# Kernel optimization log

Measured on AMD Instinct MI355X. Metric: run time of the kernel, lower is better.

The kernel has to match this reference:

```python
import jax, jax.numpy as jnp
import numpy as np

TEMPS = (0.02, 0.05, 0.2)
EPS = 1e-06


def _pairwise_dist_sq(x, y):
    # (N, M) squared L2 distances, clamped at 0 like the torch version
    dsq = (x * x).sum(-1)[:, None] + (y * y).sum(-1)[None, :] - 2.0 * (x @ y.T)
    return jnp.maximum(dsq, 0.0)


def reference(gen_features, pos_features, drift_scales):
    gen, pos = gen_features, pos_features
    N = gen.shape[0]
    # Distances are temperature-independent; compute once and reuse across temps.
    d_att = jnp.sqrt(_pairwise_dist_sq(gen, pos))  # (N_gen, N_pos)
    eye = jnp.eye(N, dtype=bool)
    dsq_rep = _pairwise_dist_sq(gen, gen)
    # diagonal gets masked to -inf in the logits anyway; replace 0 before sqrt for numerical safety
    d_rep = jnp.sqrt(jnp.where(eye, 1.0, dsq_rep))  # (N_gen, N_gen)

    drift_sum = jnp.zeros_like(gen)
    for i, T in enumerate(TEMPS):
        # attraction: sum_j softmax(-d/T)_ij * (pos_j - gen_i) == softmax @ pos - gen
        # (weights sum to 1 along axis=1, so the -gen_i term factors out)
        w_att = jax.nn.softmax(-d_att / T, axis=1)
        attraction = w_att @ pos - gen
        # repulsion: self-pair excluded via -inf logit (masked_fill(inf) on distances)
        logits_rep = jnp.where(eye, -jnp.inf, -d_rep / T)
        w_rep = jax.nn.softmax(logits_rep, axis=1)
        repulsion = w_rep @ gen - gen
        scale = jnp.maximum(drift_scales[i], EPS)
        drift_sum = drift_sum + (attraction - repulsion) / scale
    return drift_sum / len(TEMPS)


def setup_inputs() -> dict:
    key = jax.random.key(0)
    k1, k2 = jax.random.split(key)
    return {
        "gen_features": jax.random.normal(k1, (8192, 1024), dtype=jnp.float32),
        "pos_features": jax.random.normal(k2, (8192, 1024), dtype=jnp.float32),
        "drift_scales": jnp.ones((3,), dtype=jnp.float32),
    }
```

## Files before the change

kernel.cpp:

```cpp
#include <hip/hip_runtime.h>
#include <hip/hip_bf16.h>

#define NN 8192
#define DD 1024
#define KK 16384

using half8 = __attribute__((ext_vector_type(8))) _Float16;
using half4 = __attribute__((ext_vector_type(4))) _Float16;
using f32x4 = __attribute__((ext_vector_type(4))) float;

__device__ __align__(16) _Float16 g_gh[(size_t)NN * DD];
__device__ __align__(16) _Float16 g_ph[(size_t)NN * DD];
__device__ __align__(16) _Float16 g_vt[(size_t)DD * KK];
__device__ float g_gn[NN];
__device__ float g_pn[NN];
__device__ float g_datt[(size_t)NN * NN];
__device__ float g_drep[(size_t)NN * NN];
__device__ __align__(16) _Float16 g_w[(size_t)NN * KK];
__device__ float g_part[2 * (size_t)NN * DD];

typedef const __attribute__((address_space(1))) void GV;
typedef __attribute__((address_space(3))) void LV;
__device__ inline void gload16(const void* g, void* l) {
    __builtin_amdgcn_global_load_lds((GV*)g, (LV*)l, 16, 0, 0);
}

__global__ __launch_bounds__(256) void k_conv(const float* __restrict__ gen,
                                              const float* __restrict__ pos) {
    int b = blockIdx.x;
    int r = b & (NN - 1);
    const float* src = (b < NN) ? gen : pos;
    _Float16* dsth = (b < NN) ? g_gh : g_ph;
    float* dstn = (b < NN) ? g_gn : g_pn;
    int t = threadIdx.x;
    const float4* s4 = (const float4*)(src + (size_t)r * DD);
    float4 x = s4[t];
    half4 h = {(_Float16)x.x, (_Float16)x.y, (_Float16)x.z, (_Float16)x.w};
    *(half4*)(dsth + (size_t)r * DD + t * 4) = h;
    float s = x.x * x.x + x.y * x.y + x.z * x.z + x.w * x.w;
#pragma unroll
    for (int off = 32; off; off >>= 1) s += __shfl_xor(s, off);
    __shared__ float red[4];
    if ((t & 63) == 0) red[t >> 6] = s;
    __syncthreads();
    if (t == 0) dstn[r] = red[0] + red[1] + red[2] + red[3];
}

__global__ __launch_bounds__(256) void k_tr(const float* __restrict__ pos,
                                            const float* __restrict__ gen) {
    int jt = blockIdx.x;
    int dt = blockIdx.y;
    int z = blockIdx.z;
    const float* src = z ? gen : pos;
    size_t cbase = z ? (size_t)NN : 0;
    __shared__ _Float16 tile[64][68];
    int t = threadIdx.x;
    int j0 = jt * 64, d0 = dt * 64;
#pragma unroll
    for (int p = 0; p < 4; p++) {
        int idx = t + p * 256;
        int r = idx >> 4;
        int c4 = idx & 15;
        float4 x = *(const float4*)(src + (size_t)(j0 + r) * DD + d0 + c4 * 4);
        tile[r][c4 * 4 + 0] = (_Float16)x.x;
        tile[r][c4 * 4 + 1] = (_Float16)x.y;
        tile[r][c4 * 4 + 2] = (_Float16)x.z;
        tile[r][c4 * 4 + 3] = (_Float16)x.w;
    }
    __syncthreads();
#pragma unroll
    for (int p = 0; p < 4; p++) {
        int idx = t + p * 256;
        int d = idx >> 4;
        int j4 = idx & 15;
        half4 h = {tile[j4 * 4 + 0][d], tile[j4 * 4 + 1][d],
                   tile[j4 * 4 + 2][d], tile[j4 * 4 + 3][d]};
        *(half4*)(g_vt + (size_t)(d0 + d) * KK + cbase + j0 + j4 * 4) = h;
    }
}

#define MFMA16(A_, B_, C_) __builtin_amdgcn_mfma_f32_16x16x32_f16(A_, B_, C_, 0, 0, 0)
#define BAR() __builtin_amdgcn_s_barrier()
#define LGKM0() do { asm volatile("s_waitcnt lgkmcnt(0)" ::: "memory"); \
                     __builtin_amdgcn_sched_barrier(0); } while (0)
#define VM4() asm volatile("s_waitcnt vmcnt(4)" ::: "memory")
#define VM0() asm volatile("s_waitcnt vmcnt(0)" ::: "memory")

template <int LDK>
__device__ inline void gemm_core(const _Float16* __restrict__ A,
                                 const _Float16* __restrict__ B,
                                 int arow0, int brow0, int kcol0, int ntiles,
                                 _Float16* lds, f32x4 acc[8][4]) {
    int t = threadIdx.x;
    int w = t >> 6, lane = t & 63;
    int wm = w >> 2, wn = w & 3;
    int q = lane >> 4, li = lane & 15;
    _Float16* sA = lds;
    _Float16* sB = lds + 4 * 8192;

    int offA[8], offB[4];
#pragma unroll
    for (int m = 0; m < 8; ++m) {
        int row = wm * 128 + m * 16 + li;
        offA[m] = row * 32 + (q ^ ((row >> 1) & 3)) * 8;
    }
#pragma unroll
    for (int n = 0; n < 4; ++n) {
        int row = wn * 64 + n * 16 + li;
        offB[n] = row * 32 + (q ^ ((row >> 1) & 3)) * 8;
    }

    int rbase = w * 16 + (lane >> 2);
    int csrc = (lane & 3) ^ ((rbase >> 1) & 3);
    const _Float16* gA0 = A + (size_t)(arow0 + rbase) * LDK + kcol0 + csrc * 8;
    const _Float16* gA1 = gA0 + (size_t)128 * LDK;
    const _Float16* gB0 = B + (size_t)(brow0 + rbase) * LDK + kcol0 + csrc * 8;
    const _Float16* gB1 = gB0 + (size_t)128 * LDK;
    int ldst = w * 512;

#define STAGE_A(tile_) do { \
    gload16(gA0 + (size_t)(tile_) * 32, sA + ((tile_) & 3) * 8192 + ldst); \
    gload16(gA1 + (size_t)(tile_) * 32, sA + ((tile_) & 3) * 8192 + 4096 + ldst); } while (0)
#define STAGE_B(tile_) do { \
    gload16(gB0 + (size_t)(tile_) * 32, sB + ((tile_) & 3) * 8192 + ldst); \
    gload16(gB1 + (size_t)(tile_) * 32, sB + ((tile_) & 3) * 8192 + 4096 + ldst); } while (0)

    STAGE_A(0); STAGE_B(0); STAGE_A(1); STAGE_B(1);
    VM4();
    BAR();

    int nwin = ntiles >> 1;
    half8 af[4], bf[4], af2[4];
#pragma unroll 2
    for (int wi = 0; wi < nwin; ++wi) {
        int t0 = 2 * wi, t1 = t0 + 1;
        const _Float16* a0 = sA + (t0 & 3) * 8192;
        const _Float16* b0 = sB + (t0 & 3) * 8192;
        const _Float16* a1 = sA + (t1 & 3) * 8192;
        const _Float16* b1 = sB + (t1 & 3) * 8192;
#pragma unroll
        for (int m = 0; m < 4; ++m) af[m] = *(const half8*)(a0 + offA[m]);
#pragma unroll
        for (int n = 0; n < 4; ++n) bf[n] = *(const half8*)(b0 + offB[n]);
        if (t0 + 2 < ntiles) STAGE_A(t0 + 2);
        BAR();
        LGKM0();
        __builtin_amdgcn_s_setprio(1);
#pragma unroll
        for (int m = 0; m < 4; ++m)
#pragma unroll
            for (int n = 0; n < 4; ++n)
                acc[m][n] = MFMA16(af[m], bf[n], acc[m][n]);
        __builtin_amdgcn_s_setprio(0);
        BAR();
#pragma unroll
        for (int m = 0; m < 4; ++m) af2[m] = *(const half8*)(a0 + offA[m + 4]);
        if (t0 + 2 < ntiles) STAGE_B(t0 + 2);
        BAR();
        LGKM0();
        __builtin_amdgcn_s_setprio(1);
#pragma unroll
        for (int m = 0; m < 4; ++m)
#pragma unroll
            for (int n = 0; n < 4; ++n)
                acc[m + 4][n] = MFMA16(af2[m], bf[n], acc[m + 4][n]);
        __builtin_amdgcn_s_setprio(0);
        if (wi < nwin - 1) VM4(); else VM0();
        BAR();
#pragma unroll
        for (int m = 0; m < 4; ++m) af[m] = *(const half8*)(a1 + offA[m]);
#pragma unroll
        for (int n = 0; n < 4; ++n) bf[n] = *(const half8*)(b1 + offB[n]);
        if (t1 + 2 < ntiles) STAGE_A(t1 + 2);
        BAR();
        LGKM0();
        __builtin_amdgcn_s_setprio(1);
#pragma unroll
        for (int m = 0; m < 4; ++m)
#pragma unroll
            for (int n = 0; n < 4; ++n)
                acc[m][n] = MFMA16(af[m], bf[n], acc[m][n]);
        __builtin_amdgcn_s_setprio(0);
        BAR();
#pragma unroll
        for (int m = 0; m < 4; ++m) af2[m] = *(const half8*)(a1 + offA[m + 4]);
        if (t1 + 2 < ntiles) STAGE_B(t1 + 2);
        BAR();
        LGKM0();
        __builtin_amdgcn_s_setprio(1);
#pragma unroll
        for (int m = 0; m < 4; ++m)
#pragma unroll
            for (int n = 0; n < 4; ++n)
                acc[m + 4][n] = MFMA16(af2[m], bf[n], acc[m + 4][n]);
        __builtin_amdgcn_s_setprio(0);
        if (wi < nwin - 1) {
            VM4();
            BAR();
        }
    }
#undef STAGE_A
#undef STAGE_B
}

__global__ __launch_bounds__(512, 2) void k_qk2() {
    extern __shared__ _Float16 lds[];
    int id = blockIdx.y * 32 + blockIdx.x;
    id = (id & 7) * 128 + (id >> 3);
    int rt = id >> 5, ct = id & 31;
    int rep = blockIdx.z;
    const _Float16* A = g_gh;
    const _Float16* B = rep ? g_gh : g_ph;
    const float* An = g_gn;
    const float* Bn = rep ? g_gn : g_pn;
    float* outp = rep ? g_drep : g_datt;

    f32x4 acc[8][4] = {};
    gemm_core<DD>(A, B, rt * 256, ct * 256, 0, DD / 32, lds, acc);

    int t = threadIdx.x, w = t >> 6, lane = t & 63;
    int wm = w >> 2, wn = w & 3, q = lane >> 4, li = lane & 15;
    float bnv[4];
#pragma unroll
    for (int n = 0; n < 4; ++n) bnv[n] = Bn[ct * 256 + wn * 64 + n * 16 + li];
#pragma unroll
    for (int m = 0; m < 8; ++m) {
        int gi0 = rt * 256 + wm * 128 + m * 16 + q * 4;
#pragma unroll
        for (int r = 0; r < 4; ++r) {
            int gi = gi0 + r;
            float an = An[gi];
            float* orow = outp + (size_t)gi * NN;
#pragma unroll
            for (int n = 0; n < 4; ++n) {
                int gj = ct * 256 + wn * 64 + n * 16 + li;
                float dsq = an + bnv[n] - 2.0f * acc[m][n][r];
                float d = sqrtf(fmaxf(dsq, 0.0f));
                if (rep && gi == gj) d = 1e30f;
                orow[gj] = d;
            }
        }
    }
}

__global__ __launch_bounds__(256) void k_sw(const float* __restrict__ scales) {
    int i = blockIdx.x, t = threadIdx.x;
    const float4* ra = (const float4*)(g_datt + (size_t)i * NN);
    const float4* rr = (const float4*)(g_drep + (size_t)i * NN);
    float va[32], vr[32];
    float mna = 1e30f, mnr = 1e30f;
#pragma unroll
    for (int p = 0; p < 8; ++p) {
        float4 x = ra[t + p * 256];
        float4 y = rr[t + p * 256];
        va[p * 4 + 0] = x.x; va[p * 4 + 1] = x.y; va[p * 4 + 2] = x.z; va[p * 4 + 3] = x.w;
        vr[p * 4 + 0] = y.x; vr[p * 4 + 1] = y.y; vr[p * 4 + 2] = y.z; vr[p * 4 + 3] = y.w;
        mna = fminf(mna, fminf(fminf(x.x, x.y), fminf(x.z, x.w)));
        mnr = fminf(mnr, fminf(fminf(y.x, y.y), fminf(y.z, y.w)));
    }
#pragma unroll
    for (int off = 32; off; off >>= 1) {
        mna = fminf(mna, __shfl_xor(mna, off));
        mnr = fminf(mnr, __shfl_xor(mnr, off));
    }
    __shared__ float sm[2][4];
    __shared__ float ss[6][4];
    int wv = t >> 6;
    if ((t & 63) == 0) { sm[0][wv] = mna; sm[1][wv] = mnr; }
    __syncthreads();
    mna = fminf(fminf(sm[0][0], sm[0][1]), fminf(sm[0][2], sm[0][3]));
    mnr = fminf(fminf(sm[1][0], sm[1][1]), fminf(sm[1][2], sm[1][3]));
    float s0 = 0.f, s1 = 0.f, s2 = 0.f, s3 = 0.f, s4 = 0.f, s5 = 0.f;
#pragma unroll
    for (int k = 0; k < 32; ++k) {
        float da = va[k] - mna;
        s0 += __expf(da * -50.0f); s1 += __expf(da * -20.0f); s2 += __expf(da * -5.0f);
        float dr = vr[k] - mnr;
        s3 += __expf(dr * -50.0f); s4 += __expf(dr * -20.0f); s5 += __expf(dr * -5.0f);
    }
#pragma unroll
    for (int off = 32; off; off >>= 1) {
        s0 += __shfl_xor(s0, off); s1 += __shfl_xor(s1, off); s2 += __shfl_xor(s2, off);
        s3 += __shfl_xor(s3, off); s4 += __shfl_xor(s4, off); s5 += __shfl_xor(s5, off);
    }
    if ((t & 63) == 0) {
        ss[0][wv] = s0; ss[1][wv] = s1; ss[2][wv] = s2;
        ss[3][wv] = s3; ss[4][wv] = s4; ss[5][wv] = s5;
    }
    __syncthreads();
    float l0 = ss[0][0] + ss[0][1] + ss[0][2] + ss[0][3];
    float l1 = ss[1][0] + ss[1][1] + ss[1][2] + ss[1][3];
    float l2 = ss[2][0] + ss[2][1] + ss[2][2] + ss[2][3];
    float l3 = ss[3][0] + ss[3][1] + ss[3][2] + ss[3][3];
    float l4 = ss[4][0] + ss[4][1] + ss[4][2] + ss[4][3];
    float l5 = ss[5][0] + ss[5][1] + ss[5][2] + ss[5][3];
    float i0 = 1.0f / (3.0f * fmaxf(scales[0], 1e-6f));
    float i1 = 1.0f / (3.0f * fmaxf(scales[1], 1e-6f));
    float i2 = 1.0f / (3.0f * fmaxf(scales[2], 1e-6f));
    float ca0 = i0 / l0, ca1 = i1 / l1, ca2 = i2 / l2;
    float cr0 = -i0 / l3, cr1 = -i1 / l4, cr2 = -i2 / l5;
    _Float16* wa = g_w + (size_t)i * KK;
    _Float16* wr = wa + NN;
#pragma unroll
    for (int p = 0; p < 8; ++p) {
        half4 ha, hr;
#pragma unroll
        for (int qq = 0; qq < 4; ++qq) {
            float da = va[p * 4 + qq] - mna;
            ha[qq] = (_Float16)(ca0 * __expf(da * -50.0f) + ca1 * __expf(da * -20.0f) +
                                ca2 * __expf(da * -5.0f));
            float dr = vr[p * 4 + qq] - mnr;
            hr[qq] = (_Float16)(cr0 * __expf(dr * -50.0f) + cr1 * __expf(dr * -20.0f) +
                                cr2 * __expf(dr * -5.0f));
        }
        *(half4*)(wa + (size_t)(t + p * 256) * 4) = ha;
        *(half4*)(wr + (size_t)(t + p * 256) * 4) = hr;
    }
}

__global__ __launch_bounds__(512, 2) void k_gemm2() {
    extern __shared__ _Float16 lds[];
    int id = blockIdx.y * 4 + blockIdx.x;
    id = (id & 7) * 16 + (id >> 3);
    int rt = id >> 2, ct = id & 3;
    int z = blockIdx.z;
    f32x4 acc[8][4] = {};
    gemm_core<KK>(g_w, g_vt, rt * 256, ct * 256, z * (KK / 2), (KK / 2) / 32, lds, acc);
    float* outp = g_part + (size_t)z * NN * DD;
    int t = threadIdx.x, w = t >> 6, lane = t & 63;
    int wm = w >> 2, wn = w & 3, q = lane >> 4, li = lane & 15;
#pragma unroll
    for (int m = 0; m < 8; ++m) {
#pragma unroll
        for (int r = 0; r < 4; ++r) {
            int gi = rt * 256 + wm * 128 + m * 16 + q * 4 + r;
            float* orow = outp + (size_t)gi * DD;
#pragma unroll
            for (int n = 0; n < 4; ++n) {
                int gj = ct * 256 + wn * 64 + n * 16 + li;
                orow[gj] = acc[m][n][r];
            }
        }
    }
}

__global__ __launch_bounds__(256) void k_red(float* __restrict__ out) {
    size_t base = (size_t)blockIdx.x * 256 + threadIdx.x;
    const float4* p0 = (const float4*)g_part;
    const float4* p1 = (const float4*)(g_part + (size_t)NN * DD);
    float4* o4 = (float4*)out;
#pragma unroll
    for (int p = 0; p < 4; ++p) {
        size_t idx = base + (size_t)p * 524288;
        float4 a = p0[idx], b = p1[idx];
        float4 c = {a.x + b.x, a.y + b.y, a.z + b.z, a.w + b.w};
        o4[idx] = c;
    }
}

extern "C" void kernel_launch(void* const* d_in, const int* in_sizes, int n_in,
                              void* d_out, int out_size, void* d_ws, size_t ws_size,
                              hipStream_t stream) {
    (void)in_sizes; (void)n_in; (void)d_ws; (void)ws_size; (void)out_size;
    const float* gen = (const float*)d_in[0];
    const float* pos = (const float*)d_in[1];
    const float* scales = (const float*)d_in[2];

    hipFuncSetAttribute((const void*)k_qk2, hipFuncAttributeMaxDynamicSharedMemorySize, 131072);
    hipFuncSetAttribute((const void*)k_gemm2, hipFuncAttributeMaxDynamicSharedMemorySize, 131072);

    k_conv<<<dim3(2 * NN), 256, 0, stream>>>(gen, pos);
    k_tr<<<dim3(128, 16, 2), 256, 0, stream>>>(pos, gen);
    k_qk2<<<dim3(32, 32, 2), 512, 131072, stream>>>();
    k_sw<<<dim3(NN), 256, 0, stream>>>(scales);
    k_gemm2<<<dim3(4, 32, 2), 512, 131072, stream>>>();
    k_red<<<dim3(2048), 256, 0, stream>>>((float*)d_out);
}
```

Baseline: 898.3 us.

## Store distance matrices as 16-bit fixed point staged through LDS with nontemporal stores

The distance matrices passed between the QK kernel and the softmax-weight kernel are now quantized to unsigned 16-bit fixed point (scale 1024) instead of fp32. This halves the dominant intermediate traffic of two 8192x8192 matrices. The tiles are staged in LDS so global writes become coalesced 16-byte rows. The weight kernel reads and writes with wider vectors and nontemporal hints. The quantization adds rounding of about 1/2048 on distances, and values above about 64 saturate; both can distort the sharp T=0.02 softmax.

```diff
diff --git a/kernel.cpp b/kernel.cpp
--- a/kernel.cpp
+++ b/kernel.cpp
@@ -8,14 +8,15 @@
 using half8 = __attribute__((ext_vector_type(8))) _Float16;
 using half4 = __attribute__((ext_vector_type(4))) _Float16;
 using f32x4 = __attribute__((ext_vector_type(4))) float;
+using u32x4 = __attribute__((ext_vector_type(4))) unsigned int;
 
 __device__ __align__(16) _Float16 g_gh[(size_t)NN * DD];
 __device__ __align__(16) _Float16 g_ph[(size_t)NN * DD];
 __device__ __align__(16) _Float16 g_vt[(size_t)DD * KK];
 __device__ float g_gn[NN];
 __device__ float g_pn[NN];
-__device__ float g_datt[(size_t)NN * NN];
-__device__ float g_drep[(size_t)NN * NN];
+__device__ __align__(16) unsigned short g_datt[(size_t)NN * NN];
+__device__ __align__(16) unsigned short g_drep[(size_t)NN * NN];
 __device__ __align__(16) _Float16 g_w[(size_t)NN * KK];
 __device__ float g_part[2 * (size_t)NN * DD];
 
@@ -213,50 +214,70 @@
     const _Float16* B = rep ? g_gh : g_ph;
     const float* An = g_gn;
     const float* Bn = rep ? g_gn : g_pn;
-    float* outp = rep ? g_drep : g_datt;
+    unsigned short* outp = rep ? g_drep : g_datt;
 
     f32x4 acc[8][4] = {};
     gemm_core<DD>(A, B, rt * 256, ct * 256, 0, DD / 32, lds, acc);
+    __syncthreads();
 
     int t = threadIdx.x, w = t >> 6, lane = t & 63;
     int wm = w >> 2, wn = w & 3, q = lane >> 4, li = lane & 15;
+    unsigned short* sd = (unsigned short*)lds;
     float bnv[4];
 #pragma unroll
     for (int n = 0; n < 4; ++n) bnv[n] = Bn[ct * 256 + wn * 64 + n * 16 + li];
 #pragma unroll
     for (int m = 0; m < 8; ++m) {
-        int gi0 = rt * 256 + wm * 128 + m * 16 + q * 4;
+        int row0 = wm * 128 + m * 16 + q * 4;
 #pragma unroll
         for (int r = 0; r < 4; ++r) {
-            int gi = gi0 + r;
-            float an = An[gi];
-            float* orow = outp + (size_t)gi * NN;
+            int row = row0 + r;
+            float an = An[rt * 256 + row];
 #pragma unroll
             for (int n = 0; n < 4; ++n) {
-                int gj = ct * 256 + wn * 64 + n * 16 + li;
+                int col = wn * 64 + n * 16 + li;
                 float dsq = an + bnv[n] - 2.0f * acc[m][n][r];
                 float d = sqrtf(fmaxf(dsq, 0.0f));
-                if (rep && gi == gj) d = 1e30f;
-                orow[gj] = d;
+                if (rep && (rt * 256 + row) == (ct * 256 + col)) d = 1e30f;
+                float dv = fminf(d * 1024.0f + 0.5f, 65535.0f);
+                sd[row * 256 + col] = (unsigned short)(int)dv;
             }
         }
+    }
+    __syncthreads();
+    const u32x4* s4 = (const u32x4*)sd;
+    int row16 = t >> 5, chunk = t & 31;
+#pragma unroll
+    for (int i = 0; i < 16; ++i) {
+        int lrow = i * 16 + row16;
+        u32x4 v = s4[lrow * 32 + chunk];
+        u32x4* gp = (u32x4*)(outp + (size_t)(rt * 256 + lrow) * NN + ct * 256) + chunk;
+        __builtin_nontemporal_store(v, gp);
     }
 }
 
 __global__ __launch_bounds__(256) void k_sw(const float* __restrict__ scales) {
     int i = blockIdx.x, t = threadIdx.x;
-    const float4* ra = (const float4*)(g_datt + (size_t)i * NN);
-    const float4* rr = (const float4*)(g_drep + (size_t)i * NN);
+    const u32x4* ra = (const u32x4*)(g_datt + (size_t)i * NN);
+    const u32x4* rr = (const u32x4*)(g_drep + (size_t)i * NN);
     float va[32], vr[32];
     float mna = 1e30f, mnr = 1e30f;
-#pragma unroll
-    for (int p = 0; p < 8; ++p) {
-        float4 x = ra[t + p * 256];
-        float4 y = rr[t + p * 256];
-        va[p * 4 + 0] = x.x; va[p * 4 + 1] = x.y; va[p * 4 + 2] = x.z; va[p * 4 + 3] = x.w;
-        vr[p * 4 + 0] = y.x; vr[p * 4 + 1] = y.y; vr[p * 4 + 2] = y.z; vr[p * 4 + 3] = y.w;
-        mna = fminf(mna, fminf(fminf(x.x, x.y), fminf(x.z, x.w)));
-        mnr = fminf(mnr, fminf(fminf(y.x, y.y), fminf(y.z, y.w)));
+    const float SC = 1.0f / 1024.0f;
+#pragma unroll
+    for (int p = 0; p < 4; ++p) {
+        u32x4 x = __builtin_nontemporal_load(&ra[t + p * 256]);
+        u32x4 y = __builtin_nontemporal_load(&rr[t + p * 256]);
+#pragma unroll
+        for (int u = 0; u < 4; ++u) {
+            float a0 = (float)(x[u] & 0xFFFFu) * SC;
+            float a1 = (float)(x[u] >> 16) * SC;
+            float r0 = (float)(y[u] & 0xFFFFu) * SC;
+            float r1 = (float)(y[u] >> 16) * SC;
+            va[p * 8 + u * 2 + 0] = a0; va[p * 8 + u * 2 + 1] = a1;
+            vr[p * 8 + u * 2 + 0] = r0; vr[p * 8 + u * 2 + 1] = r1;
+            mna = fminf(mna, fminf(a0, a1));
+            mnr = fminf(mnr, fminf(r0, r1));
+        }
     }
 #pragma unroll
     for (int off = 32; off; off >>= 1) {
@@ -302,19 +323,19 @@
     _Float16* wa = g_w + (size_t)i * KK;
     _Float16* wr = wa + NN;
 #pragma unroll
-    for (int p = 0; p < 8; ++p) {
-        half4 ha, hr;
-#pragma unroll
-        for (int qq = 0; qq < 4; ++qq) {
-            float da = va[p * 4 + qq] - mna;
-            ha[qq] = (_Float16)(ca0 * __expf(da * -50.0f) + ca1 * __expf(da * -20.0f) +
-                                ca2 * __expf(da * -5.0f));
-            float dr = vr[p * 4 + qq] - mnr;
-            hr[qq] = (_Float16)(cr0 * __expf(dr * -50.0f) + cr1 * __expf(dr * -20.0f) +
-                                cr2 * __expf(dr * -5.0f));
-        }
-        *(half4*)(wa + (size_t)(t + p * 256) * 4) = ha;
-        *(half4*)(wr + (size_t)(t + p * 256) * 4) = hr;
+    for (int p = 0; p < 4; ++p) {
+        union { half8 h; u32x4 u; } ha, hr;
+#pragma unroll
+        for (int qq = 0; qq < 8; ++qq) {
+            float da = va[p * 8 + qq] - mna;
+            ha.h[qq] = (_Float16)(ca0 * __expf(da * -50.0f) + ca1 * __expf(da * -20.0f) +
+                                  ca2 * __expf(da * -5.0f));
+            float dr = vr[p * 8 + qq] - mnr;
+            hr.h[qq] = (_Float16)(cr0 * __expf(dr * -50.0f) + cr1 * __expf(dr * -20.0f) +
+                                  cr2 * __expf(dr * -5.0f));
+        }
+        __builtin_nontemporal_store(ha.u, (u32x4*)(wa + (size_t)(t + p * 256) * 8));
+        __builtin_nontemporal_store(hr.u, (u32x4*)(wr + (size_t)(t + p * 256) * 8));
     }
 }
 
@@ -366,8 +387,8 @@
     const float* pos = (const float*)d_in[1];
     const float* scales = (const float*)d_in[2];
 
-    hipFuncSetAttribute((const void*)k_qk2, hipFuncAttributeMaxDynamicSharedMemorySize, 131072);
-    hipFuncSetAttribute((const void*)k_gemm2, hipFuncAttributeMaxDynamicSharedMemorySize, 131072);
+    (void)hipFuncSetAttribute((const void*)k_qk2, hipFuncAttributeMaxDynamicSharedMemorySize, 131072);
+    (void)hipFuncSetAttribute((const void*)k_gemm2, hipFuncAttributeMaxDynamicSharedMemorySize, 131072);
 
     k_conv<<<dim3(2 * NN), 256, 0, stream>>>(gen, pos);
     k_tr<<<dim3(128, 16, 2), 256, 0, stream>>>(pos, gen);
```

Result: faster. 832.2 us (-7.4%).
